# Optimization experiments

Measured on AMD Instinct MI355X. Metric: run time of the kernel, lower is better.

## Reference

```python
import jax, jax.numpy as jnp
import numpy as np

E, H, L = 512, 1024, 2
SRC_V, TGT_V = 32000, 32000
B, S, T = 32, 128, 128
BOS = 1  # vocab.Vocab.bos_idx


def _lstm_layer(x, h0, c0, Wih, Whh, bih, bhh):
    """Single-direction LSTM layer. x: [B, S, D] -> (ys [B,S,H], hT, cT).
    PyTorch gate order: i, f, g, o."""
    b = bih + bhh
    def step(carry, xt):
        h, c = carry
        gates = xt @ Wih.T + h @ Whh.T + b          # [B, 4H]
        i, f, g, o = jnp.split(gates, 4, axis=-1)
        i = jax.nn.sigmoid(i)
        f = jax.nn.sigmoid(f)
        g = jnp.tanh(g)
        o = jax.nn.sigmoid(o)
        c = f * c + i * g
        h = o * jnp.tanh(c)
        return (h, c), h
    (hT, cT), ys = jax.lax.scan(step, (h0, c0), jnp.swapaxes(x, 0, 1))
    return jnp.swapaxes(ys, 0, 1), hT, cT


def _stacked_lstm(x, h0s, c0s, params):
    """params: list of (Wih, Whh, bih, bhh) per layer. h0s/c0s: [L, B, H]."""
    hs, cs = [], []
    y = x
    for l, (Wih, Whh, bih, bhh) in enumerate(params):
        y, hT, cT = _lstm_layer(y, h0s[l], c0s[l], Wih, Whh, bih, bhh)
        hs.append(hT)
        cs.append(cT)
    return y, jnp.stack(hs), jnp.stack(cs)


def setup_inputs() -> dict:
    key = jax.random.key(0)
    ks = jax.random.split(key, 24)
    sc = 1.0 / np.sqrt(H)
    inp = {}
    inp["src"] = jax.random.randint(ks[0], (B, S), 0, SRC_V)
    inp["tgt"] = jax.random.randint(ks[1], (B, T), 0, TGT_V)
    inp["enc_emb"] = jax.random.normal(ks[2], (SRC_V, E), jnp.float32)
    inp["dec_emb"] = jax.random.normal(ks[3], (TGT_V, E), jnp.float32)
    i = 4
    for pre in ("enc", "dec"):
        for l in range(L):
            din = E if l == 0 else H
            inp[f"{pre}_Wih{l}"] = jax.random.uniform(ks[i + 0], (4 * H, din), jnp.float32, -sc, sc)
            inp[f"{pre}_Whh{l}"] = jax.random.uniform(ks[i + 1], (4 * H, H), jnp.float32, -sc, sc)
            inp[f"{pre}_bih{l}"] = jax.random.uniform(ks[i + 2], (4 * H,), jnp.float32, -sc, sc)
            inp[f"{pre}_bhh{l}"] = jax.random.uniform(ks[i + 3], (4 * H,), jnp.float32, -sc, sc)
            i += 4
    return inp


def reference(src, tgt, enc_emb, dec_emb,
              enc_Wih0, enc_Whh0, enc_bih0, enc_bhh0,
              enc_Wih1, enc_Whh1, enc_bih1, enc_bhh1,
              dec_Wih0, dec_Whh0, dec_bih0, dec_bhh0,
              dec_Wih1, dec_Whh1, dec_bih1, dec_bhh1):
    enc_params = [(enc_Wih0, enc_Whh0, enc_bih0, enc_bhh0),
                  (enc_Wih1, enc_Whh1, enc_bih1, enc_bhh1)]
    dec_params = [(dec_Wih0, dec_Whh0, dec_bih0, dec_bhh0),
                  (dec_Wih1, dec_Whh1, dec_bih1, dec_bhh1)]
    # Encoder: full-sequence LSTM from zero state
    x = enc_emb[src]                                  # [B, S, E]
    zeros = jnp.zeros((L, B, H), x.dtype)
    enc_out, h, c = _stacked_lstm(x, zeros, zeros, enc_params)
    # Decoder: teacher-forced inputs = [BOS, tgt[:, :-1]]
    dec_in = jnp.concatenate(
        [jnp.full((B, 1), BOS, tgt.dtype), tgt[:, :-1]], axis=1)  # [B, T]
    y = dec_emb[dec_in]                               # [B, T, E]
    dec_out, _, _ = _stacked_lstm(y, h, c, dec_params)
    return dec_out                                    # [B, T, H]
```

## Files before the change

### kernel.cpp

```cpp
#include <hip/hip_runtime.h>
#include <hip/hip_bf16.h>
#include <stdint.h>


typedef __attribute__((ext_vector_type(8))) __bf16 bf16x8;
typedef __attribute__((ext_vector_type(4))) __bf16 bf16x4;
typedef __attribute__((ext_vector_type(4))) float  f32x4;

#define SLAB 32768
#define RNN_SMEM (65536 + 65536 + 512)

__device__ __forceinline__ float sigmoidf_(float x) {
  return 1.f / (1.f + __expf(-x));
}
__device__ __forceinline__ float tanhf_(float x) {
  float e = __expf(-2.f * fabsf(x));
  float t = (1.f - e) / (1.f + e);
  return x < 0.f ? -t : t;
}

__global__ void init_ws(float* zeros, unsigned* flags) {
  int i = blockIdx.x * 256 + threadIdx.x;
  if (i < 32 * 1024) zeros[i] = 0.f;
  if (i < 512) flags[i] = 0u;
}

__global__ void gather_emb(const int* __restrict__ src, const int* __restrict__ tgt,
                           const float* __restrict__ ee, const float* __restrict__ de,
                           __bf16* __restrict__ Xe, __bf16* __restrict__ Xd) {
  int row = blockIdx.x & 4095;
  int t = row >> 5, b = row & 31;
  bool isd = blockIdx.x >= 4096;
  int tok = isd ? (t == 0 ? 1 : tgt[b * 128 + t - 1]) : src[b * 128 + t];
  const float* ep = (isd ? de : ee) + (size_t)tok * 512;
  __bf16* op = (isd ? Xd : Xe) + (size_t)row * 512;
  int i = threadIdx.x * 4;
  float4 v = *(const float4*)(ep + i);
  bf16x4 t4;
  t4[0] = (__bf16)v.x; t4[1] = (__bf16)v.y; t4[2] = (__bf16)v.z; t4[3] = (__bf16)v.w;
  *(bf16x4*)(op + i) = t4;
}

__global__ __launch_bounds__(256) void gemm_xp(
    const __bf16* __restrict__ A, const float* __restrict__ W,
    const float* __restrict__ bih, const float* __restrict__ bhh,
    __bf16* __restrict__ C, int K) {
  __shared__ char sA[128 * 64 * 2];
  __shared__ char sB[128 * 64 * 2];
  int tid = threadIdx.x;
  int lane = tid & 63, wave = tid >> 6;
  int wm = wave & 1, wn = wave >> 1;
  int bm = blockIdx.x & 31, bn = blockIdx.x >> 5;
  int frow = lane & 15;
  int kj = (lane >> 4) * 16;

  f32x4 acc[4][4] = {};

  for (int k0 = 0; k0 < K; k0 += 64) {
#pragma unroll
    for (int c4 = 0; c4 < 4; ++c4) {
      int idx = (c4 * 256 + tid) * 8;
      int r = idx >> 6, kk = idx & 63;
      bf16x8 v = *(const bf16x8*)(A + (size_t)(bm * 128 + r) * K + k0 + kk);
      *(bf16x8*)(sA + ((r * 128 + kk * 2) ^ ((r & 7) << 4))) = v;
    }
#pragma unroll
    for (int c4 = 0; c4 < 4; ++c4) {
      int idx = (c4 * 256 + tid) * 8;
      int r = idx >> 6, kk = idx & 63;
      const float* wp = W + (size_t)(bn * 128 + r) * K + k0 + kk;
      float4 w0 = *(const float4*)wp;
      float4 w1 = *(const float4*)(wp + 4);
      bf16x8 v;
      v[0] = (__bf16)w0.x; v[1] = (__bf16)w0.y; v[2] = (__bf16)w0.z; v[3] = (__bf16)w0.w;
      v[4] = (__bf16)w1.x; v[5] = (__bf16)w1.y; v[6] = (__bf16)w1.z; v[7] = (__bf16)w1.w;
      *(bf16x8*)(sB + ((r * 128 + kk * 2) ^ ((r & 7) << 4))) = v;
    }
    __syncthreads();
#pragma unroll
    for (int half = 0; half < 2; ++half) {
      int kb = half * 64 + kj;
      bf16x8 af[4], bfr[4];
#pragma unroll
      for (int f = 0; f < 4; ++f) {
        int arr = wm * 64 + f * 16 + frow;
        af[f] = *(const bf16x8*)(sA + (arr * 128 + (kb ^ ((arr & 7) << 4))));
        int brr = wn * 64 + f * 16 + frow;
        bfr[f] = *(const bf16x8*)(sB + (brr * 128 + (kb ^ ((brr & 7) << 4))));
      }
#pragma unroll
      for (int fm = 0; fm < 4; ++fm)
#pragma unroll
        for (int fn = 0; fn < 4; ++fn)
          acc[fm][fn] = __builtin_amdgcn_mfma_f32_16x16x32_bf16(af[fm], bfr[fn],
                                                                acc[fm][fn], 0, 0, 0);
    }
    __syncthreads();
  }
  int cm = bm * 128 + wm * 64, cn = bn * 128 + wn * 64;
#pragma unroll
  for (int fn = 0; fn < 4; ++fn) {
    int col = cn + fn * 16 + frow;
    int g = col >> 10, hcol = col & 1023;
    int blkd = hcol >> 3, hl = hcol & 7;
    float bias = bih[col] + bhh[col];
#pragma unroll
    for (int fm = 0; fm < 4; ++fm) {
      int r0 = cm + fm * 16 + ((lane >> 4) << 2);
#pragma unroll
      for (int j = 0; j < 4; ++j) {
        int row = r0 + j;
        C[(size_t)(row >> 5) * 131072 + blkd * 1024 + hl * 128 + g * 32 +
          (row & 31)] = (__bf16)(acc[fm][fn][j] + bias);
      }
    }
  }
}

struct RnnArgs {
  const float* Whh;
  const float* Wxh;
  const float* bih;
  const float* bhh;
  const __bf16* XP;
  const __bf16* xslab;
  const unsigned* xflags;
  const __bf16* h0;
  const float* c0;
  __bf16* hseq;
  float* cfin;
  float* yout;
  unsigned* flags;
};

__device__ __forceinline__ f32x4 accum_k1024_sw(f32x4 acc, const char* bbase,
                                                const char* aRow, int swz, int kj) {
#pragma unroll
  for (int kt = 0; kt < 32; kt += 8) {
    bf16x8 bv[8];
#pragma unroll
    for (int u = 0; u < 8; ++u)
      bv[u] = *(const bf16x8*)(bbase + (size_t)(kt + u) * 2048);
#pragma unroll
    for (int u = 0; u < 8; ++u) {
      int kb = (kt + u) * 64 + kj;
      bf16x8 av = *(const bf16x8*)(aRow + (kb ^ swz));
      acc = __builtin_amdgcn_mfma_f32_16x16x32_bf16(av, bv[u], acc, 0, 0, 0);
    }
  }
  return acc;
}

__device__ __forceinline__ void rnn_body(const RnnArgs& P, int blk, char* smem) {
  char*   sW0 = smem;
  char*   sW1 = smem + 65536;
  __bf16* sP  = (__bf16*)(smem + 131072);

  int tid = threadIdx.x;
  int lane = tid & 63, wave = tid >> 6;
  int mt = wave & 1, nt = wave >> 1;
  bool isL0 = (P.XP != nullptr);

  __builtin_amdgcn_fence(__ATOMIC_ACQUIRE, "agent");

  {
    const float* srcs[2] = {P.Wxh, P.Whh};
    char* dsts[2] = {sW0, sW1};
    for (int s = (isL0 ? 1 : 0); s < 2; ++s) {
      for (int g = 0; g < 4; ++g) {
        const float* sp = srcs[s] + (size_t)(g * 1024 + blk * 8) * 1024;
#pragma unroll
        for (int it = 0; it < 8; ++it) {
          int e = (it * 256 + tid) * 4;
          int rl = e >> 10, k = e & 1023;
          float4 v = *(const float4*)(sp + e);
          bf16x4 t4;
          t4[0] = (__bf16)v.x; t4[1] = (__bf16)v.y;
          t4[2] = (__bf16)v.z; t4[3] = (__bf16)v.w;
          int r = rl * 4 + g;
          *(bf16x4*)(dsts[s] + ((r << 11) + ((k << 1) ^ ((r & 7) << 4)))) = t4;
        }
      }
    }
  }

  int hl = mt * 4 + (lane >> 4);
  int b  = nt * 16 + (lane & 15);
  float c = P.c0[b * 1024 + blk * 8 + hl];

  float bI = 0.f, bF = 0.f, bG = 0.f, bO = 0.f;
  if (!isL0) {
    int col = blk * 8 + hl;
    bI = P.bih[col] + P.bhh[col];
    bF = P.bih[1024 + col] + P.bhh[1024 + col];
    bG = P.bih[2048 + col] + P.bhh[2048 + col];
    bO = P.bih[3072 + col] + P.bhh[3072 + col];
  }

  int rr  = mt * 16 + (lane & 15);
  int swz = (rr & 7) << 4;
  const char* aRow0 = sW0 + (rr << 11);
  const char* aRow1 = sW1 + (rr << 11);
  int kj   = (lane >> 4) * 16;
  int bsub = (lane >> 4) * 512 + b * 16;

  const __bf16* xpb = isL0 ? (P.XP + (size_t)blk * 1024 + hl * 128 + b) : nullptr;

  for (int t = 0; t < 128; ++t) {
    float xi = bI, xf = bF, xg = bG, xo = bO;
    if (isL0) {
      const __bf16* xr = xpb + (size_t)t * 131072;
      xi = (float)xr[0];  xf = (float)xr[32];
      xg = (float)xr[64]; xo = (float)xr[96];
    }

    if (wave == 0 && (t > 0 || !isL0)) {
      unsigned th = (unsigned)t, tx = (unsigned)(t + 1);
      for (;;) {
        bool ok = true;
        if (!isL0)
          ok = (__hip_atomic_load(P.xflags + lane, __ATOMIC_RELAXED,
                                  __HIP_MEMORY_SCOPE_AGENT) >= tx) &&
               (__hip_atomic_load(P.xflags + 64 + lane, __ATOMIC_RELAXED,
                                  __HIP_MEMORY_SCOPE_AGENT) >= tx);
        if (t > 0)
          ok = ok &&
               (__hip_atomic_load(P.flags + lane, __ATOMIC_RELAXED,
                                  __HIP_MEMORY_SCOPE_AGENT) >= th) &&
               (__hip_atomic_load(P.flags + 64 + lane, __ATOMIC_RELAXED,
                                  __HIP_MEMORY_SCOPE_AGENT) >= th);
        if (__all(ok)) break;
        __builtin_amdgcn_s_sleep(1);
      }
    }
    __syncthreads();

    const char* hb = (const char*)((t == 0) ? P.h0
                                            : (P.hseq + (size_t)(t - 1) * SLAB)) + bsub;
    f32x4 acc = {0.f, 0.f, 0.f, 0.f};
    if (!isL0) {
      const char* xb = (const char*)(P.xslab + (size_t)t * SLAB) + bsub;
      acc = accum_k1024_sw(acc, xb, aRow0, swz, kj);
    }
    acc = accum_k1024_sw(acc, hb, aRow1, swz, kj);

    float gi = sigmoidf_(acc[0] + xi);
    float gf = sigmoidf_(acc[1] + xf);
    float gg = tanhf_(acc[2] + xg);
    float go = sigmoidf_(acc[3] + xo);
    c = gf * c + gi * gg;
    float h = go * tanhf_(c);
    sP[b * 8 + hl] = (__bf16)h;
    __syncthreads();

    if (tid < 64) {
      unsigned long long v = *(const unsigned long long*)(sP + tid * 4);
      unsigned long long* dst = (unsigned long long*)(
          (char*)P.hseq + (size_t)t * 65536 + blk * 512 + tid * 8);
      __hip_atomic_store(dst, v, __ATOMIC_RELAXED, __HIP_MEMORY_SCOPE_AGENT);
      asm volatile("s_waitcnt vmcnt(0)" ::: "memory");
      if (tid == 0)
        __hip_atomic_store(P.flags + blk, (unsigned)(t + 1), __ATOMIC_RELEASE,
                           __HIP_MEMORY_SCOPE_AGENT);
    }
    if (P.yout) {
      int yb = tid >> 3, yhl = tid & 7;
      P.yout[((size_t)yb * 128 + t) * 1024 + blk * 8 + yhl] =
          (float)sP[yb * 8 + yhl];
    }
  }
  P.cfin[b * 1024 + blk * 8 + hl] = c;
}

__global__ __launch_bounds__(256) void rnn_pair(RnnArgs A, RnnArgs B) {
  extern __shared__ char smem[];
  if (blockIdx.x < 128) rnn_body(A, blockIdx.x, smem);
  else                  rnn_body(B, blockIdx.x - 128, smem);
}

extern "C" void kernel_launch(void* const* d_in, const int* in_sizes, int n_in,
                              void* d_out, int out_size, void* d_ws, size_t ws_size,
                              hipStream_t stream) {
  (void)in_sizes; (void)n_in; (void)out_size; (void)ws_size;
  const int*   src     = (const int*)d_in[0];
  const int*   tgt     = (const int*)d_in[1];
  const float* enc_emb = (const float*)d_in[2];
  const float* dec_emb = (const float*)d_in[3];
  const float* W[16];
  for (int i = 0; i < 16; ++i) W[i] = (const float*)d_in[4 + i];

  char* ws = (char*)d_ws;
  size_t off = 0;
  auto alloc = [&](size_t bytes) {
    char* p = ws + off;
    off += (bytes + 255) & ~(size_t)255;
    return p;
  };
  unsigned* flags = (unsigned*)alloc((size_t)4 * 128 * sizeof(unsigned));
  float*    zeros = (float*)alloc((size_t)32 * 1024 * 4);
  __bf16*   Xe   = (__bf16*)alloc((size_t)4096 * 512 * 2);
  __bf16*   Xd   = (__bf16*)alloc((size_t)4096 * 512 * 2);
  __bf16*   XP1  = (__bf16*)alloc((size_t)4096 * 4096 * 2);
  __bf16*   XP2  = (__bf16*)alloc((size_t)4096 * 4096 * 2);
  __bf16*   hE0  = (__bf16*)alloc((size_t)128 * SLAB * 2);
  __bf16*   hE1  = (__bf16*)alloc((size_t)128 * SLAB * 2);
  __bf16*   hD0  = (__bf16*)alloc((size_t)128 * SLAB * 2);
  __bf16*   hD1  = (__bf16*)alloc((size_t)128 * SLAB * 2);
  float*    cE0  = (float*)alloc((size_t)32 * 1024 * 4);
  float*    cE1  = (float*)alloc((size_t)32 * 1024 * 4);
  float*    cd0  = (float*)alloc((size_t)32 * 1024 * 4);
  float*    cd1  = (float*)alloc((size_t)32 * 1024 * 4);

  hipFuncSetAttribute((const void*)rnn_pair,
                      hipFuncAttributeMaxDynamicSharedMemorySize, RNN_SMEM);

  init_ws<<<128, 256, 0, stream>>>(zeros, flags);
  gather_emb<<<8192, 128, 0, stream>>>(src, tgt, enc_emb, dec_emb, Xe, Xd);

  gemm_xp<<<1024, 256, 0, stream>>>(Xe, W[0], W[2], W[3], XP1, 512);
  gemm_xp<<<1024, 256, 0, stream>>>(Xd, W[8], W[10], W[11], XP2, 512);

  unsigned* fE0 = flags;
  unsigned* fE1 = flags + 128;
  unsigned* fD0 = flags + 256;
  unsigned* fD1 = flags + 384;

  RnnArgs e0{W[1], nullptr, nullptr, nullptr, XP1, nullptr, nullptr,
             (const __bf16*)zeros, zeros, hE0, cE0, nullptr, fE0};
  RnnArgs e1{W[5], W[4], W[6], W[7], nullptr, hE0, fE0,
             (const __bf16*)zeros, zeros, hE1, cE1, nullptr, fE1};
  rnn_pair<<<256, 256, RNN_SMEM, stream>>>(e0, e1);

  RnnArgs d0{W[9], nullptr, nullptr, nullptr, XP2, nullptr, nullptr,
             hE0 + (size_t)127 * SLAB, cE0, hD0, cd0, nullptr, fD0};
  RnnArgs d1{W[13], W[12], W[14], W[15], nullptr, hD0, fD0,
             hE1 + (size_t)127 * SLAB, cE1, hD1, cd1, (float*)d_out, fD1};
  rnn_pair<<<256, 256, RNN_SMEM, stream>>>(d0, d1);
}
```

Baseline: 2.193 ms.

## Add dedicated sync wave for flag polling and prefetch all recurrent operands

Adds a fifth wave per block whose only job is to spin on the cross-block step flags, so the four compute waves no longer share a wave with the poller. The k-loop is restructured to issue all 32 (or 64) global bf16x8 loads of x/h up front before the MFMA chain, replacing the 8-deep batched load/MFMA groups. This trades higher register pressure (launch_bounds 320,1) and an idle extra wave for deeper memory-level parallelism on the per-step latency-bound recurrence.

After: 2.605 ms. 18.8% more time.

```diff
diff --git a/kernel.cpp b/kernel.cpp
--- a/kernel.cpp
+++ b/kernel.cpp
@@ -133,24 +133,6 @@
   unsigned* flags;
 };
 
-__device__ __forceinline__ f32x4 accum_k1024_sw(f32x4 acc, const char* bbase,
-                                                const char* aRow, int swz, int kj) {
-#pragma unroll
-  for (int kt = 0; kt < 32; kt += 8) {
-    bf16x8 bv[8];
-#pragma unroll
-    for (int u = 0; u < 8; ++u)
-      bv[u] = *(const bf16x8*)(bbase + (size_t)(kt + u) * 2048);
-#pragma unroll
-    for (int u = 0; u < 8; ++u) {
-      int kb = (kt + u) * 64 + kj;
-      bf16x8 av = *(const bf16x8*)(aRow + (kb ^ swz));
-      acc = __builtin_amdgcn_mfma_f32_16x16x32_bf16(av, bv[u], acc, 0, 0, 0);
-    }
-  }
-  return acc;
-}
-
 __device__ __forceinline__ void rnn_body(const RnnArgs& P, int blk, char* smem) {
   char*   sW0 = smem;
   char*   sW1 = smem + 65536;
@@ -158,12 +140,13 @@
 
   int tid = threadIdx.x;
   int lane = tid & 63, wave = tid >> 6;
-  int mt = wave & 1, nt = wave >> 1;
+  bool syncw = (wave == 4);
+  int mt = wave & 1, nt = (wave >> 1) & 1;
   bool isL0 = (P.XP != nullptr);
 
   __builtin_amdgcn_fence(__ATOMIC_ACQUIRE, "agent");
 
-  {
+  if (tid < 256) {
     const float* srcs[2] = {P.Wxh, P.Whh};
     char* dsts[2] = {sW0, sW1};
     for (int s = (isL0 ? 1 : 0); s < 2; ++s) {
@@ -186,10 +169,11 @@
 
   int hl = mt * 4 + (lane >> 4);
   int b  = nt * 16 + (lane & 15);
-  float c = P.c0[b * 1024 + blk * 8 + hl];
+  float c = 0.f;
+  if (!syncw) c = P.c0[b * 1024 + blk * 8 + hl];
 
   float bI = 0.f, bF = 0.f, bG = 0.f, bO = 0.f;
-  if (!isL0) {
+  if (!isL0 && !syncw) {
     int col = blk * 8 + hl;
     bI = P.bih[col] + P.bhh[col];
     bF = P.bih[1024 + col] + P.bhh[1024 + col];
@@ -204,53 +188,86 @@
   int kj   = (lane >> 4) * 16;
   int bsub = (lane >> 4) * 512 + b * 16;
 
-  const __bf16* xpb = isL0 ? (P.XP + (size_t)blk * 1024 + hl * 128 + b) : nullptr;
+  const __bf16* xpb = (isL0 && !syncw)
+                          ? (P.XP + (size_t)blk * 1024 + hl * 128 + b) : nullptr;
 
   for (int t = 0; t < 128; ++t) {
+    if (syncw) {
+      if (t > 0 || !isL0) {
+        unsigned th = (unsigned)t, tx = (unsigned)(t + 1);
+        for (;;) {
+          bool ok = true;
+          if (!isL0)
+            ok = (__hip_atomic_load(P.xflags + lane, __ATOMIC_RELAXED,
+                                    __HIP_MEMORY_SCOPE_AGENT) >= tx) &&
+                 (__hip_atomic_load(P.xflags + 64 + lane, __ATOMIC_RELAXED,
+                                    __HIP_MEMORY_SCOPE_AGENT) >= tx);
+          if (t > 0)
+            ok = ok &&
+                 (__hip_atomic_load(P.flags + lane, __ATOMIC_RELAXED,
+                                    __HIP_MEMORY_SCOPE_AGENT) >= th) &&
+                 (__hip_atomic_load(P.flags + 64 + lane, __ATOMIC_RELAXED,
+                                    __HIP_MEMORY_SCOPE_AGENT) >= th);
+          if (__all(ok)) break;
+          __builtin_amdgcn_s_sleep(1);
+        }
+      }
+    }
+
     float xi = bI, xf = bF, xg = bG, xo = bO;
-    if (isL0) {
+    if (isL0 && !syncw) {
       const __bf16* xr = xpb + (size_t)t * 131072;
       xi = (float)xr[0];  xf = (float)xr[32];
       xg = (float)xr[64]; xo = (float)xr[96];
     }
 
-    if (wave == 0 && (t > 0 || !isL0)) {
-      unsigned th = (unsigned)t, tx = (unsigned)(t + 1);
-      for (;;) {
-        bool ok = true;
-        if (!isL0)
-          ok = (__hip_atomic_load(P.xflags + lane, __ATOMIC_RELAXED,
-                                  __HIP_MEMORY_SCOPE_AGENT) >= tx) &&
-               (__hip_atomic_load(P.xflags + 64 + lane, __ATOMIC_RELAXED,
-                                  __HIP_MEMORY_SCOPE_AGENT) >= tx);
-        if (t > 0)
-          ok = ok &&
-               (__hip_atomic_load(P.flags + lane, __ATOMIC_RELAXED,
-                                  __HIP_MEMORY_SCOPE_AGENT) >= th) &&
-               (__hip_atomic_load(P.flags + 64 + lane, __ATOMIC_RELAXED,
-                                  __HIP_MEMORY_SCOPE_AGENT) >= th);
-        if (__all(ok)) break;
-        __builtin_amdgcn_s_sleep(1);
-      }
-    }
     __syncthreads();
 
-    const char* hb = (const char*)((t == 0) ? P.h0
-                                            : (P.hseq + (size_t)(t - 1) * SLAB)) + bsub;
-    f32x4 acc = {0.f, 0.f, 0.f, 0.f};
-    if (!isL0) {
-      const char* xb = (const char*)(P.xslab + (size_t)t * SLAB) + bsub;
-      acc = accum_k1024_sw(acc, xb, aRow0, swz, kj);
-    }
-    acc = accum_k1024_sw(acc, hb, aRow1, swz, kj);
-
-    float gi = sigmoidf_(acc[0] + xi);
-    float gf = sigmoidf_(acc[1] + xf);
-    float gg = tanhf_(acc[2] + xg);
-    float go = sigmoidf_(acc[3] + xo);
-    c = gf * c + gi * gg;
-    float h = go * tanhf_(c);
-    sP[b * 8 + hl] = (__bf16)h;
+    if (!syncw) {
+      f32x4 acc = {0.f, 0.f, 0.f, 0.f};
+      const char* hb = (const char*)((t == 0) ? P.h0
+                         : (P.hseq + (size_t)(t - 1) * SLAB)) + bsub;
+      if (!isL0) {
+        const char* xb = (const char*)(P.xslab + (size_t)t * SLAB) + bsub;
+        bf16x8 xv[32], hv[32];
+#pragma unroll
+        for (int u = 0; u < 32; ++u)
+          xv[u] = *(const bf16x8*)(xb + (size_t)u * 2048);
+#pragma unroll
+        for (int u = 0; u < 32; ++u)
+          hv[u] = *(const bf16x8*)(hb + (size_t)u * 2048);
+#pragma unroll
+        for (int u = 0; u < 32; ++u) {
+          int kb = u * 64 + kj;
+          bf16x8 av = *(const bf16x8*)(aRow0 + (kb ^ swz));
+          acc = __builtin_amdgcn_mfma_f32_16x16x32_bf16(av, xv[u], acc, 0, 0, 0);
+        }
+#pragma unroll
+        for (int u = 0; u < 32; ++u) {
+          int kb = u * 64 + kj;
+          bf16x8 av = *(const bf16x8*)(aRow1 + (kb ^ swz));
+          acc = __builtin_amdgcn_mfma_f32_16x16x32_bf16(av, hv[u], acc, 0, 0, 0);
+        }
+      } else {
+        bf16x8 hv[32];
+#pragma unroll
+        for (int u = 0; u < 32; ++u)
+          hv[u] = *(const bf16x8*)(hb + (size_t)u * 2048);
+#pragma unroll
+        for (int u = 0; u < 32; ++u) {
+          int kb = u * 64 + kj;
+          bf16x8 av = *(const bf16x8*)(aRow1 + (kb ^ swz));
+          acc = __builtin_amdgcn_mfma_f32_16x16x32_bf16(av, hv[u], acc, 0, 0, 0);
+        }
+      }
+      float gi = sigmoidf_(acc[0] + xi);
+      float gf = sigmoidf_(acc[1] + xf);
+      float gg = tanhf_(acc[2] + xg);
+      float go = sigmoidf_(acc[3] + xo);
+      c = gf * c + gi * gg;
+      float h = go * tanhf_(c);
+      sP[b * 8 + hl] = (__bf16)h;
+    }
     __syncthreads();
 
     if (tid < 64) {
@@ -263,16 +280,16 @@
         __hip_atomic_store(P.flags + blk, (unsigned)(t + 1), __ATOMIC_RELEASE,
                            __HIP_MEMORY_SCOPE_AGENT);
     }
-    if (P.yout) {
+    if (P.yout && tid < 256) {
       int yb = tid >> 3, yhl = tid & 7;
       P.yout[((size_t)yb * 128 + t) * 1024 + blk * 8 + yhl] =
           (float)sP[yb * 8 + yhl];
     }
   }
-  P.cfin[b * 1024 + blk * 8 + hl] = c;
-}
-
-__global__ __launch_bounds__(256) void rnn_pair(RnnArgs A, RnnArgs B) {
+  if (!syncw) P.cfin[b * 1024 + blk * 8 + hl] = c;
+}
+
+__global__ __launch_bounds__(320, 1) void rnn_pair(RnnArgs A, RnnArgs B) {
   extern __shared__ char smem[];
   if (blockIdx.x < 128) rnn_body(A, blockIdx.x, smem);
   else                  rnn_body(B, blockIdx.x - 128, smem);
@@ -329,11 +346,11 @@
              (const __bf16*)zeros, zeros, hE0, cE0, nullptr, fE0};
   RnnArgs e1{W[5], W[4], W[6], W[7], nullptr, hE0, fE0,
              (const __bf16*)zeros, zeros, hE1, cE1, nullptr, fE1};
-  rnn_pair<<<256, 256, RNN_SMEM, stream>>>(e0, e1);
+  rnn_pair<<<256, 320, RNN_SMEM, stream>>>(e0, e1);
 
   RnnArgs d0{W[9], nullptr, nullptr, nullptr, XP2, nullptr, nullptr,
              hE0 + (size_t)127 * SLAB, cE0, hD0, cd0, nullptr, fD0};
   RnnArgs d1{W[13], W[12], W[14], W[15], nullptr, hD0, fD0,
              hE1 + (size_t)127 * SLAB, cE1, hD1, cd1, (float*)d_out, fD1};
-  rnn_pair<<<256, 256, RNN_SMEM, stream>>>(d0, d1);
-}
+  rnn_pair<<<256, 320, RNN_SMEM, stream>>>(d0, d1);
+}
```
